# Optimization experiments

Hardware: AMD Instinct MI355X
Metric: run time of the kernel (lower is better)

## Reference

```python
import math
import jax, jax.numpy as jnp
import numpy as np

TOP_K = 2
_GELU_C = math.sqrt(2.0 / math.pi)

def gelu_new(x):
    # NewGELU: tanh approximation identical to the torch module
    return 0.5 * x * (1.0 + jnp.tanh(_GELU_C * (x + 0.044715 * x * x * x)))

def setup_inputs() -> dict:
    key = jax.random.key(0)
    ks = jax.random.split(key, 6)
    B, T, C, E, H = 2, 2048, 1024, 8, 4096
    s_in = 1.0 / math.sqrt(C)
    s_hid = 1.0 / math.sqrt(H)
    return {
        "x": jax.random.normal(ks[0], (B, T, C), dtype=jnp.float32),
        "router_w": jax.random.normal(ks[1], (E, C), dtype=jnp.float32) * s_in,
        "w_fc": jax.random.normal(ks[2], (E, C, H), dtype=jnp.float32) * s_in,
        "b_fc": jax.random.normal(ks[3], (E, H), dtype=jnp.float32) * 0.02,
        "w_proj": jax.random.normal(ks[4], (E, H, C), dtype=jnp.float32) * s_hid,
        "b_proj": jax.random.normal(ks[5], (E, C), dtype=jnp.float32) * 0.02,
    }

def reference(x, router_w, w_fc, b_fc, w_proj, b_proj):
    B, T, C = x.shape
    E = router_w.shape[0]
    N = B * T
    xf = x.reshape(N, C)
    # Router: Linear(C, E, bias=False), softmax, top-k, renormalize
    logits = xf @ router_w.T                              # [N, E]
    probs = jax.nn.softmax(logits, axis=-1)
    topk_probs, topk_idx = jax.lax.top_k(probs, TOP_K)    # [N, K]
    topk_probs = topk_probs / jnp.sum(topk_probs, axis=-1, keepdims=True)
    # Dense combine weights: zero for unselected experts -> same math as
    # gather/FFN/index_add over selected tokens (dropout=0).
    combine = jnp.zeros((N, E), dtype=x.dtype).at[
        jnp.arange(N)[:, None], topk_idx].add(topk_probs)  # [N, E]
    # Expert FFN applied per expert (batched GEMMs)
    h = gelu_new(jnp.einsum('nc,ech->neh', xf, w_fc) + b_fc)      # [N, E, H]
    out = jnp.einsum('neh,ehc->nec', h, w_proj) + b_proj          # [N, E, C]
    y = jnp.einsum('nec,ne->nc', out, combine)                    # [N, C]
    return y.reshape(B, T, C)
```

## Files before the change

kernel.cpp:

```cpp
#include <hip/hip_runtime.h>
#include <hip/hip_bf16.h>


#define NTOK  4096
#define CDIM  1024
#define HDIM  4096
#define NEXP  8
#define NPC   9216
#define MAXMT 72
#define LDK   40

typedef _Float16 half8 __attribute__((ext_vector_type(8)));
typedef float    f32x4 __attribute__((ext_vector_type(4)));

__device__ __forceinline__ float gelu_new(float x) {
    const float c = 0.7978845608028654f;
    return 0.5f * x * (1.0f + tanhf(c * (x + 0.044715f * x * x * x)));
}


__global__ void zero_u32(unsigned int* __restrict__ p, int n) {
    int i = blockIdx.x * 256 + threadIdx.x;
    if (i < n) p[i] = 0u;
}

__global__ void cvt_x_kernel(const float* __restrict__ x, _Float16* __restrict__ xh) {
    int i = (blockIdx.x * 256 + threadIdx.x) * 8;
    float4 a = *(const float4*)(x + i);
    float4 b = *(const float4*)(x + i + 4);
    half8 o;
    o[0] = (_Float16)a.x; o[1] = (_Float16)a.y; o[2] = (_Float16)a.z; o[3] = (_Float16)a.w;
    o[4] = (_Float16)b.x; o[5] = (_Float16)b.y; o[6] = (_Float16)b.z; o[7] = (_Float16)b.w;
    *(half8*)(xh + i) = o;
}


__global__ __launch_bounds__(256) void router_kernel(
    const float* __restrict__ x, const float* __restrict__ rw,
    int* __restrict__ tok_e, float* __restrict__ tok_w, int* __restrict__ counts)
{
    int wave = threadIdx.x >> 6, lane = threadIdx.x & 63;
    int n = blockIdx.x * 4 + wave;
    const float* xr = x + (size_t)n * CDIM;
    float acc[NEXP];
    #pragma unroll
    for (int e = 0; e < NEXP; ++e) acc[e] = 0.f;
    for (int c = lane; c < CDIM; c += 64) {
        float xv = xr[c];
        #pragma unroll
        for (int e = 0; e < NEXP; ++e) acc[e] = fmaf(xv, rw[e * CDIM + c], acc[e]);
    }
    #pragma unroll
    for (int e = 0; e < NEXP; ++e) {
        float v = acc[e];
        #pragma unroll
        for (int off = 32; off > 0; off >>= 1) v += __shfl_down(v, off);
        acc[e] = v;
    }
    if (lane == 0) {
        float l0 = -3.0e38f, l1 = -3.0e38f; int b0 = 0, b1 = 0;
        #pragma unroll
        for (int e = 0; e < NEXP; ++e) {
            float v = acc[e];
            if (v > l0)      { l1 = l0; b1 = b0; l0 = v; b0 = e; }
            else if (v > l1) { l1 = v; b1 = e; }
        }
        float t  = __expf(l1 - l0) ;
        t = expf(l1 - l0);
        float w0 = 1.f / (1.f + t);
        float w1 = t  / (1.f + t);
        tok_e[n * 2]     = b0;  tok_e[n * 2 + 1] = b1;
        tok_w[n * 2]     = w0;  tok_w[n * 2 + 1] = w1;
        atomicAdd(&counts[b0], 1);
        atomicAdd(&counts[b1], 1);
    }
}

__global__ void plan_kernel(const int* __restrict__ counts, int* __restrict__ cursors,
                            int* __restrict__ mtiles, int* __restrict__ tile_expert)
{
    if (threadIdx.x == 0 && blockIdx.x == 0) {
        int b = 0;
        for (int e = 0; e < NEXP; ++e) {
            cursors[e] = b;
            int tiles = (counts[e] + 127) >> 7;
            for (int t = 0; t < tiles; ++t) tile_expert[(b >> 7) + t] = e;
            b += tiles << 7;
        }
        *mtiles = b >> 7;
        for (int t = b >> 7; t < MAXMT; ++t) tile_expert[t] = 0;
    }
}

__global__ void assign_kernel(const int* __restrict__ tok_e, const float* __restrict__ tok_w,
                              int* __restrict__ cursors,
                              int* __restrict__ pair_tok, float* __restrict__ pair_gate)
{
    int n = blockIdx.x * 256 + threadIdx.x;
    #pragma unroll
    for (int k = 0; k < 2; ++k) {
        int e = tok_e[n * 2 + k];
        int slot = atomicAdd(&cursors[e], 1);
        pair_tok[slot]  = n;
        pair_gate[slot] = tok_w[n * 2 + k];
    }
}


__global__ __launch_bounds__(256) void gemm_fc_kernel(
    const _Float16* __restrict__ xh,
    const float*    __restrict__ w_fc,
    const float*    __restrict__ b_fc,
    const int*      __restrict__ pair_tok,
    const int*      __restrict__ tile_expert,
    const int*      __restrict__ mtiles,
    _Float16*       __restrict__ hb)
{
    const int mt = blockIdx.y;
    if (mt >= *mtiles) return;
    const int nt = blockIdx.x;
    const int e  = tile_expert[mt];
    const int m0 = mt << 7, n0 = nt << 7;

    __shared__ _Float16 As[128 * LDK];
    __shared__ _Float16 Bs[128 * LDK];

    const int tid = threadIdx.x;
    const int lane = tid & 63, wv = tid >> 6;
    const int wm = (wv >> 1) * 64, wn = (wv & 1) * 64;
    const int l16 = lane & 15, lq = lane >> 4;

    const int arow = tid >> 2;
    const int ach  = (tid & 3) * 8;
    const int tok0 = pair_tok[m0 + arow];
    const int tok1 = pair_tok[m0 + arow + 64];
    const _Float16* asrc0 = xh + (size_t)tok0 * CDIM + ach;
    const _Float16* asrc1 = xh + (size_t)tok1 * CDIM + ach;

    const int nloc = tid & 127;
    const int kg   = (tid >> 7) * 16;
    const float* bsrc = w_fc + ((size_t)e * CDIM + kg) * HDIM + n0 + nloc;

    f32x4 acc[4][4];
    #pragma unroll
    for (int i = 0; i < 4; ++i)
        #pragma unroll
        for (int j = 0; j < 4; ++j) { acc[i][j][0]=0.f; acc[i][j][1]=0.f; acc[i][j][2]=0.f; acc[i][j][3]=0.f; }

    for (int k0 = 0; k0 < CDIM; k0 += 32) {
        *(half8*)&As[arow * LDK + ach]        = *(const half8*)(asrc0 + k0);
        *(half8*)&As[(arow + 64) * LDK + ach] = *(const half8*)(asrc1 + k0);
        const float* bs = bsrc + (size_t)k0 * HDIM;
        #pragma unroll
        for (int h = 0; h < 2; ++h) {
            half8 pk;
            #pragma unroll
            for (int j = 0; j < 8; ++j) pk[j] = (_Float16)bs[(size_t)(h * 8 + j) * HDIM];
            *(half8*)&Bs[nloc * LDK + kg + h * 8] = pk;
        }
        __syncthreads();
        half8 af[4], bfv[4];
        #pragma unroll
        for (int i = 0; i < 4; ++i) af[i]  = *(const half8*)&As[(wm + i * 16 + l16) * LDK + lq * 8];
        #pragma unroll
        for (int j = 0; j < 4; ++j) bfv[j] = *(const half8*)&Bs[(wn + j * 16 + l16) * LDK + lq * 8];
        #pragma unroll
        for (int i = 0; i < 4; ++i)
            #pragma unroll
            for (int j = 0; j < 4; ++j)
                acc[i][j] = __builtin_amdgcn_mfma_f32_16x16x32_f16(af[i], bfv[j], acc[i][j], 0, 0, 0);
        __syncthreads();
    }

    float bias[4];
    #pragma unroll
    for (int j = 0; j < 4; ++j) bias[j] = b_fc[e * HDIM + n0 + wn + j * 16 + l16];
    #pragma unroll
    for (int i = 0; i < 4; ++i) {
        #pragma unroll
        for (int r = 0; r < 4; ++r) {
            int slot = m0 + wm + i * 16 + lq * 4 + r;
            _Float16* dst = hb + (size_t)slot * HDIM + n0 + wn + l16;
            #pragma unroll
            for (int j = 0; j < 4; ++j)
                dst[j * 16] = (_Float16)gelu_new(acc[i][j][r] + bias[j]);
        }
    }
}


__global__ __launch_bounds__(256) void gemm_proj_kernel(
    const _Float16* __restrict__ hb,
    const float*    __restrict__ w_proj,
    const float*    __restrict__ b_proj,
    const int*      __restrict__ pair_tok,
    const float*    __restrict__ pair_gate,
    const int*      __restrict__ tile_expert,
    const int*      __restrict__ mtiles,
    float*          __restrict__ y)
{
    const int mt = blockIdx.y;
    if (mt >= *mtiles) return;
    const int nt = blockIdx.x;
    const int e  = tile_expert[mt];
    const int m0 = mt << 7, n0 = nt << 7;

    __shared__ _Float16 As[128 * LDK];
    __shared__ _Float16 Bs[128 * LDK];

    const int tid = threadIdx.x;
    const int lane = tid & 63, wv = tid >> 6;
    const int wm = (wv >> 1) * 64, wn = (wv & 1) * 64;
    const int l16 = lane & 15, lq = lane >> 4;

    const int arow = tid >> 2;
    const int ach  = (tid & 3) * 8;
    const _Float16* asrc0 = hb + (size_t)(m0 + arow) * HDIM + ach;
    const _Float16* asrc1 = hb + (size_t)(m0 + arow + 64) * HDIM + ach;

    const int nloc = tid & 127;
    const int kg   = (tid >> 7) * 16;
    const float* bsrc = w_proj + ((size_t)e * HDIM + kg) * CDIM + n0 + nloc;

    f32x4 acc[4][4];
    #pragma unroll
    for (int i = 0; i < 4; ++i)
        #pragma unroll
        for (int j = 0; j < 4; ++j) { acc[i][j][0]=0.f; acc[i][j][1]=0.f; acc[i][j][2]=0.f; acc[i][j][3]=0.f; }

    for (int k0 = 0; k0 < HDIM; k0 += 32) {
        *(half8*)&As[arow * LDK + ach]        = *(const half8*)(asrc0 + k0);
        *(half8*)&As[(arow + 64) * LDK + ach] = *(const half8*)(asrc1 + k0);
        const float* bs = bsrc + (size_t)k0 * CDIM;
        #pragma unroll
        for (int h = 0; h < 2; ++h) {
            half8 pk;
            #pragma unroll
            for (int j = 0; j < 8; ++j) pk[j] = (_Float16)bs[(size_t)(h * 8 + j) * CDIM];
            *(half8*)&Bs[nloc * LDK + kg + h * 8] = pk;
        }
        __syncthreads();
        half8 af[4], bfv[4];
        #pragma unroll
        for (int i = 0; i < 4; ++i) af[i]  = *(const half8*)&As[(wm + i * 16 + l16) * LDK + lq * 8];
        #pragma unroll
        for (int j = 0; j < 4; ++j) bfv[j] = *(const half8*)&Bs[(wn + j * 16 + l16) * LDK + lq * 8];
        #pragma unroll
        for (int i = 0; i < 4; ++i)
            #pragma unroll
            for (int j = 0; j < 4; ++j)
                acc[i][j] = __builtin_amdgcn_mfma_f32_16x16x32_f16(af[i], bfv[j], acc[i][j], 0, 0, 0);
        __syncthreads();
    }

    float bias[4];
    #pragma unroll
    for (int j = 0; j < 4; ++j) bias[j] = b_proj[e * CDIM + n0 + wn + j * 16 + l16];
    #pragma unroll
    for (int i = 0; i < 4; ++i) {
        #pragma unroll
        for (int r = 0; r < 4; ++r) {
            int slot = m0 + wm + i * 16 + lq * 4 + r;
            float g  = pair_gate[slot];
            if (g != 0.0f) {
                int tok = pair_tok[slot];
                float* dst = y + (size_t)tok * CDIM + n0 + wn + l16;
                #pragma unroll
                for (int j = 0; j < 4; ++j)
                    atomicAdd(&dst[j * 16], (acc[i][j][r] + bias[j]) * g);
            }
        }
    }
}


extern "C" void kernel_launch(void* const* d_in, const int* in_sizes, int n_in,
                              void* d_out, int out_size, void* d_ws, size_t ws_size,
                              hipStream_t stream) {
    const float* x   = (const float*)d_in[0];
    const float* rw  = (const float*)d_in[1];
    const float* wfc = (const float*)d_in[2];
    const float* bfc = (const float*)d_in[3];
    const float* wpj = (const float*)d_in[4];
    const float* bpj = (const float*)d_in[5];
    float* y = (float*)d_out;

    char* ws = (char*)d_ws;
    _Float16* xh        = (_Float16*)(ws);
    _Float16* hb        = (_Float16*)(ws + 8388608);
    int*      pair_tok  = (int*)     (ws + 83886080);
    float*    pair_gate = (float*)   (ws + 83922944);
    int*      tok_e     = (int*)     (ws + 83959808);
    float*    tok_w     = (float*)   (ws + 83992576);
    int*      counts    = (int*)     (ws + 84025344);
    int*      cursors   = counts + 8;
    int*      mtiles    = cursors + 8;
    int*      tile_expert = mtiles + 2;

    zero_u32<<<36, 256, 0, stream>>>((unsigned int*)pair_tok, NPC);
    zero_u32<<<36, 256, 0, stream>>>((unsigned int*)pair_gate, NPC);
    zero_u32<<<1, 256, 0, stream>>>((unsigned int*)counts, NEXP);
    zero_u32<<<16384, 256, 0, stream>>>((unsigned int*)y, NTOK * CDIM);

    cvt_x_kernel<<<2048, 256, 0, stream>>>(x, xh);
    router_kernel<<<1024, 256, 0, stream>>>(x, rw, tok_e, tok_w, counts);
    plan_kernel<<<1, 64, 0, stream>>>(counts, cursors, mtiles, tile_expert);
    assign_kernel<<<16, 256, 0, stream>>>(tok_e, tok_w, cursors, pair_tok, pair_gate);

    gemm_fc_kernel<<<dim3(HDIM / 128, MAXMT), 256, 0, stream>>>(
        xh, wfc, bfc, pair_tok, tile_expert, mtiles, hb);
    gemm_proj_kernel<<<dim3(CDIM / 128, MAXMT), 256, 0, stream>>>(
        hb, wpj, bpj, pair_tok, pair_gate, tile_expert, mtiles, y);
}
```

Before: 753.4 us.

## Pre-pack weights and gathered activations into K-blocked fp16 with async LDS loads

Result: faster. 735.7 us (-2.3%).

```diff
diff --git a/kernel.cpp b/kernel.cpp
--- a/kernel.cpp
+++ b/kernel.cpp
@@ -1,5 +1,4 @@
 #include <hip/hip_runtime.h>
-#include <hip/hip_bf16.h>
 
 
 #define NTOK  4096
@@ -8,10 +7,16 @@
 #define NEXP  8
 #define NPC   9216
 #define MAXMT 72
-#define LDK   40
+#define KB_C  32
+#define KB_H  128
 
 typedef _Float16 half8 __attribute__((ext_vector_type(8)));
 typedef float    f32x4 __attribute__((ext_vector_type(4)));
+
+#define ASYNC_CP16(gp, lp)                                                         \
+  __builtin_amdgcn_global_load_lds(                                                \
+      (const __attribute__((address_space(1))) unsigned int*)(gp),                 \
+      (__attribute__((address_space(3))) unsigned int*)(lp), 16, 0, 0)
 
 __device__ __forceinline__ float gelu_new(float x) {
     const float c = 0.7978845608028654f;
@@ -22,16 +27,6 @@
 __global__ void zero_u32(unsigned int* __restrict__ p, int n) {
     int i = blockIdx.x * 256 + threadIdx.x;
     if (i < n) p[i] = 0u;
-}
-
-__global__ void cvt_x_kernel(const float* __restrict__ x, _Float16* __restrict__ xh) {
-    int i = (blockIdx.x * 256 + threadIdx.x) * 8;
-    float4 a = *(const float4*)(x + i);
-    float4 b = *(const float4*)(x + i + 4);
-    half8 o;
-    o[0] = (_Float16)a.x; o[1] = (_Float16)a.y; o[2] = (_Float16)a.z; o[3] = (_Float16)a.w;
-    o[4] = (_Float16)b.x; o[5] = (_Float16)b.y; o[6] = (_Float16)b.z; o[7] = (_Float16)b.w;
-    *(half8*)(xh + i) = o;
 }
 
 
@@ -65,8 +60,7 @@
             if (v > l0)      { l1 = l0; b1 = b0; l0 = v; b0 = e; }
             else if (v > l1) { l1 = v; b1 = e; }
         }
-        float t  = __expf(l1 - l0) ;
-        t = expf(l1 - l0);
+        float t  = expf(l1 - l0);
         float w0 = 1.f / (1.f + t);
         float w1 = t  / (1.f + t);
         tok_e[n * 2]     = b0;  tok_e[n * 2 + 1] = b1;
@@ -107,11 +101,53 @@
 }
 
 
+__global__ __launch_bounds__(256) void gather_x_kernel(
+    const float* __restrict__ x, const int* __restrict__ pair_tok,
+    _Float16* __restrict__ xg)
+{
+    int o = blockIdx.x * 256 + threadIdx.x;
+    int kb   = o / (NPC * 4);
+    int rem  = o - kb * (NPC * 4);
+    int slot = rem >> 2;
+    int c    = (rem & 3) * 8;
+    int tok  = pair_tok[slot];
+    const float* src = x + (size_t)tok * CDIM + kb * 32 + c;
+    float4 a = *(const float4*)src;
+    float4 b = *(const float4*)(src + 4);
+    half8 h;
+    h[0] = (_Float16)a.x; h[1] = (_Float16)a.y; h[2] = (_Float16)a.z; h[3] = (_Float16)a.w;
+    h[4] = (_Float16)b.x; h[5] = (_Float16)b.y; h[6] = (_Float16)b.z; h[7] = (_Float16)b.w;
+    *(half8*)(xg + ((size_t)kb * NPC + slot) * 32 + c) = h;
+}
+
+
+__global__ __launch_bounds__(256) void transpose_cvt_kernel(
+    const float* __restrict__ w, _Float16* __restrict__ wt, int K, int N)
+{
+    __shared__ float tile[32][68];
+    const int e = blockIdx.z, k0 = blockIdx.y * 32, n0 = blockIdx.x * 64;
+    const float* src = w + ((size_t)e * K + k0) * N + n0;
+    const int t = threadIdx.x;
+    #pragma unroll
+    for (int f = t; f < 512; f += 256) {
+        int k = f >> 4, nc = (f & 15) * 4;
+        *(float4*)&tile[k][nc] = *(const float4*)(src + (size_t)k * N + nc);
+    }
+    __syncthreads();
+    int n = t >> 2, c2 = (t & 3) * 8;
+    half8 h;
+    #pragma unroll
+    for (int q = 0; q < 8; ++q) h[q] = (_Float16)tile[c2 + q][n];
+    int KB = K >> 5;
+    _Float16* dst = wt + (((size_t)e * KB + (k0 >> 5)) * N + (n0 + n)) * 32 + c2;
+    *(half8*)dst = h;
+}
+
+
 __global__ __launch_bounds__(256) void gemm_fc_kernel(
-    const _Float16* __restrict__ xh,
-    const float*    __restrict__ w_fc,
+    const _Float16* __restrict__ xg,
+    const _Float16* __restrict__ wt,
     const float*    __restrict__ b_fc,
-    const int*      __restrict__ pair_tok,
     const int*      __restrict__ tile_expert,
     const int*      __restrict__ mtiles,
     _Float16*       __restrict__ hb)
@@ -122,24 +158,19 @@
     const int e  = tile_expert[mt];
     const int m0 = mt << 7, n0 = nt << 7;
 
-    __shared__ _Float16 As[128 * LDK];
-    __shared__ _Float16 Bs[128 * LDK];
+    __shared__ _Float16 As[128 * 32];
+    __shared__ _Float16 Bs[128 * 32];
 
     const int tid = threadIdx.x;
     const int lane = tid & 63, wv = tid >> 6;
     const int wm = (wv >> 1) * 64, wn = (wv & 1) * 64;
     const int l16 = lane & 15, lq = lane >> 4;
 
-    const int arow = tid >> 2;
-    const int ach  = (tid & 3) * 8;
-    const int tok0 = pair_tok[m0 + arow];
-    const int tok1 = pair_tok[m0 + arow + 64];
-    const _Float16* asrc0 = xh + (size_t)tok0 * CDIM + ach;
-    const _Float16* asrc1 = xh + (size_t)tok1 * CDIM + ach;
-
-    const int nloc = tid & 127;
-    const int kg   = (tid >> 7) * 16;
-    const float* bsrc = w_fc + ((size_t)e * CDIM + kg) * HDIM + n0 + nloc;
+    const char* gA0 = (const char*)xg + (size_t)m0 * 64;
+    const char* gB0 = (const char*)wt + ((size_t)e * KB_C * HDIM + n0) * 64;
+    const int soff = wv * 2048 + lane * 16;
+    char* lA = (char*)As + wv * 2048;
+    char* lB = (char*)Bs + wv * 2048;
 
     f32x4 acc[4][4];
     #pragma unroll
@@ -147,23 +178,19 @@
         #pragma unroll
         for (int j = 0; j < 4; ++j) { acc[i][j][0]=0.f; acc[i][j][1]=0.f; acc[i][j][2]=0.f; acc[i][j][3]=0.f; }
 
-    for (int k0 = 0; k0 < CDIM; k0 += 32) {
-        *(half8*)&As[arow * LDK + ach]        = *(const half8*)(asrc0 + k0);
-        *(half8*)&As[(arow + 64) * LDK + ach] = *(const half8*)(asrc1 + k0);
-        const float* bs = bsrc + (size_t)k0 * HDIM;
-        #pragma unroll
-        for (int h = 0; h < 2; ++h) {
-            half8 pk;
-            #pragma unroll
-            for (int j = 0; j < 8; ++j) pk[j] = (_Float16)bs[(size_t)(h * 8 + j) * HDIM];
-            *(half8*)&Bs[nloc * LDK + kg + h * 8] = pk;
-        }
+    for (int kb = 0; kb < KB_C; ++kb) {
+        const char* ga = gA0 + (size_t)kb * (NPC * 64) + soff;
+        const char* gb = gB0 + (size_t)kb * (HDIM * 64) + soff;
+        ASYNC_CP16(ga,        lA);
+        ASYNC_CP16(ga + 1024, lA + 1024);
+        ASYNC_CP16(gb,        lB);
+        ASYNC_CP16(gb + 1024, lB + 1024);
         __syncthreads();
         half8 af[4], bfv[4];
         #pragma unroll
-        for (int i = 0; i < 4; ++i) af[i]  = *(const half8*)&As[(wm + i * 16 + l16) * LDK + lq * 8];
-        #pragma unroll
-        for (int j = 0; j < 4; ++j) bfv[j] = *(const half8*)&Bs[(wn + j * 16 + l16) * LDK + lq * 8];
+        for (int i = 0; i < 4; ++i) af[i]  = *(const half8*)&As[(wm + i * 16 + l16) * 32 + lq * 8];
+        #pragma unroll
+        for (int j = 0; j < 4; ++j) bfv[j] = *(const half8*)&Bs[(wn + j * 16 + l16) * 32 + lq * 8];
         #pragma unroll
         for (int i = 0; i < 4; ++i)
             #pragma unroll
@@ -180,10 +207,12 @@
         #pragma unroll
         for (int r = 0; r < 4; ++r) {
             int slot = m0 + wm + i * 16 + lq * 4 + r;
-            _Float16* dst = hb + (size_t)slot * HDIM + n0 + wn + l16;
             #pragma unroll
-            for (int j = 0; j < 4; ++j)
-                dst[j * 16] = (_Float16)gelu_new(acc[i][j][r] + bias[j]);
+            for (int j = 0; j < 4; ++j) {
+                int n = n0 + wn + j * 16 + l16;
+                float v = gelu_new(acc[i][j][r] + bias[j]);
+                hb[((size_t)(n >> 5) * NPC + slot) * 32 + (n & 31)] = (_Float16)v;
+            }
         }
     }
 }
@@ -191,7 +220,7 @@
 
 __global__ __launch_bounds__(256) void gemm_proj_kernel(
     const _Float16* __restrict__ hb,
-    const float*    __restrict__ w_proj,
+    const _Float16* __restrict__ wt,
     const float*    __restrict__ b_proj,
     const int*      __restrict__ pair_tok,
     const float*    __restrict__ pair_gate,
@@ -202,25 +231,23 @@
     const int mt = blockIdx.y;
     if (mt >= *mtiles) return;
     const int nt = blockIdx.x;
+    const int ks = blockIdx.z;
     const int e  = tile_expert[mt];
     const int m0 = mt << 7, n0 = nt << 7;
 
-    __shared__ _Float16 As[128 * LDK];
-    __shared__ _Float16 Bs[128 * LDK];
+    __shared__ _Float16 As[128 * 32];
+    __shared__ _Float16 Bs[128 * 32];
 
     const int tid = threadIdx.x;
     const int lane = tid & 63, wv = tid >> 6;
     const int wm = (wv >> 1) * 64, wn = (wv & 1) * 64;
     const int l16 = lane & 15, lq = lane >> 4;
 
-    const int arow = tid >> 2;
-    const int ach  = (tid & 3) * 8;
-    const _Float16* asrc0 = hb + (size_t)(m0 + arow) * HDIM + ach;
-    const _Float16* asrc1 = hb + (size_t)(m0 + arow + 64) * HDIM + ach;
-
-    const int nloc = tid & 127;
-    const int kg   = (tid >> 7) * 16;
-    const float* bsrc = w_proj + ((size_t)e * HDIM + kg) * CDIM + n0 + nloc;
+    const char* gA0 = (const char*)hb + (size_t)m0 * 64;
+    const char* gB0 = (const char*)wt + ((size_t)e * KB_H * CDIM + n0) * 64;
+    const int soff = wv * 2048 + lane * 16;
+    char* lA = (char*)As + wv * 2048;
+    char* lB = (char*)Bs + wv * 2048;
 
     f32x4 acc[4][4];
     #pragma unroll
@@ -228,23 +255,20 @@
         #pragma unroll
         for (int j = 0; j < 4; ++j) { acc[i][j][0]=0.f; acc[i][j][1]=0.f; acc[i][j][2]=0.f; acc[i][j][3]=0.f; }
 
-    for (int k0 = 0; k0 < HDIM; k0 += 32) {
-        *(half8*)&As[arow * LDK + ach]        = *(const half8*)(asrc0 + k0);
-        *(half8*)&As[(arow + 64) * LDK + ach] = *(const half8*)(asrc1 + k0);
-        const float* bs = bsrc + (size_t)k0 * CDIM;
-        #pragma unroll
-        for (int h = 0; h < 2; ++h) {
-            half8 pk;
-            #pragma unroll
-            for (int j = 0; j < 8; ++j) pk[j] = (_Float16)bs[(size_t)(h * 8 + j) * CDIM];
-            *(half8*)&Bs[nloc * LDK + kg + h * 8] = pk;
-        }
+    const int kb_end = ks * 64 + 64;
+    for (int kb = ks * 64; kb < kb_end; ++kb) {
+        const char* ga = gA0 + (size_t)kb * (NPC * 64) + soff;
+        const char* gb = gB0 + (size_t)kb * (CDIM * 64) + soff;
+        ASYNC_CP16(ga,        lA);
+        ASYNC_CP16(ga + 1024, lA + 1024);
+        ASYNC_CP16(gb,        lB);
+        ASYNC_CP16(gb + 1024, lB + 1024);
         __syncthreads();
         half8 af[4], bfv[4];
         #pragma unroll
-        for (int i = 0; i < 4; ++i) af[i]  = *(const half8*)&As[(wm + i * 16 + l16) * LDK + lq * 8];
-        #pragma unroll
-        for (int j = 0; j < 4; ++j) bfv[j] = *(const half8*)&Bs[(wn + j * 16 + l16) * LDK + lq * 8];
+        for (int i = 0; i < 4; ++i) af[i]  = *(const half8*)&As[(wm + i * 16 + l16) * 32 + lq * 8];
+        #pragma unroll
+        for (int j = 0; j < 4; ++j) bfv[j] = *(const half8*)&Bs[(wn + j * 16 + l16) * 32 + lq * 8];
         #pragma unroll
         for (int i = 0; i < 4; ++i)
             #pragma unroll
@@ -255,7 +279,8 @@
 
     float bias[4];
     #pragma unroll
-    for (int j = 0; j < 4; ++j) bias[j] = b_proj[e * CDIM + n0 + wn + j * 16 + l16];
+    for (int j = 0; j < 4; ++j)
+        bias[j] = (ks == 0) ? b_proj[e * CDIM + n0 + wn + j * 16 + l16] : 0.0f;
     #pragma unroll
     for (int i = 0; i < 4; ++i) {
         #pragma unroll
@@ -286,29 +311,34 @@
     float* y = (float*)d_out;
 
     char* ws = (char*)d_ws;
-    _Float16* xh        = (_Float16*)(ws);
-    _Float16* hb        = (_Float16*)(ws + 8388608);
-    int*      pair_tok  = (int*)     (ws + 83886080);
-    float*    pair_gate = (float*)   (ws + 83922944);
-    int*      tok_e     = (int*)     (ws + 83959808);
-    float*    tok_w     = (float*)   (ws + 83992576);
-    int*      counts    = (int*)     (ws + 84025344);
-    int*      cursors   = counts + 8;
-    int*      mtiles    = cursors + 8;
-    int*      tile_expert = mtiles + 2;
+    _Float16* xg  = (_Float16*)(ws);
+    _Float16* hb  = (_Float16*)(ws + 18874368);
+    _Float16* wt  = (_Float16*)(ws + 94371840);
+    char* meta = ws + 161480704;
+    int*   pair_tok    = (int*)  (meta);
+    float* pair_gate   = (float*)(meta + 36864);
+    int*   tok_e       = (int*)  (meta + 73728);
+    float* tok_w       = (float*)(meta + 106496);
+    int*   counts      = (int*)  (meta + 139264);
+    int*   cursors     = counts + 8;
+    int*   mtiles      = cursors + 8;
+    int*   tile_expert = mtiles + 2;
 
     zero_u32<<<36, 256, 0, stream>>>((unsigned int*)pair_tok, NPC);
     zero_u32<<<36, 256, 0, stream>>>((unsigned int*)pair_gate, NPC);
     zero_u32<<<1, 256, 0, stream>>>((unsigned int*)counts, NEXP);
     zero_u32<<<16384, 256, 0, stream>>>((unsigned int*)y, NTOK * CDIM);
 
-    cvt_x_kernel<<<2048, 256, 0, stream>>>(x, xh);
     router_kernel<<<1024, 256, 0, stream>>>(x, rw, tok_e, tok_w, counts);
     plan_kernel<<<1, 64, 0, stream>>>(counts, cursors, mtiles, tile_expert);
     assign_kernel<<<16, 256, 0, stream>>>(tok_e, tok_w, cursors, pair_tok, pair_gate);
-
+    gather_x_kernel<<<KB_C * NPC * 4 / 256, 256, 0, stream>>>(x, pair_tok, xg);
+
+    transpose_cvt_kernel<<<dim3(HDIM / 64, CDIM / 32, NEXP), 256, 0, stream>>>(wfc, wt, CDIM, HDIM);
     gemm_fc_kernel<<<dim3(HDIM / 128, MAXMT), 256, 0, stream>>>(
-        xh, wfc, bfc, pair_tok, tile_expert, mtiles, hb);
-    gemm_proj_kernel<<<dim3(CDIM / 128, MAXMT), 256, 0, stream>>>(
-        hb, wpj, bpj, pair_tok, pair_gate, tile_expert, mtiles, y);
-}
+        xg, wt, bfc, tile_expert, mtiles, hb);
+
+    transpose_cvt_kernel<<<dim3(CDIM / 64, HDIM / 32, NEXP), 256, 0, stream>>>(wpj, wt, HDIM, CDIM);
+    gemm_proj_kernel<<<dim3(CDIM / 128, MAXMT, 2), 256, 0, stream>>>(
+        hb, wt, bpj, pair_tok, pair_gate, tile_expert, mtiles, y);
+}
```
